# Optimization experiments

Measured on AMD Instinct MI355X. Metric: run time of the kernel, lower is better.

The kernel has to match this reference:

```python
import jax, jax.numpy as jnp
import numpy as np

B, S, D, H = 4, 2048, 1024, 16
DH = D // H  # depth per head


def setup_inputs() -> dict:
    key = jax.random.key(0)
    ks = jax.random.split(key, 12)
    s = 1.0 / np.sqrt(D)
    return {
        "v": jax.random.normal(ks[0], (B, S, D), jnp.float32),
        "k": jax.random.normal(ks[1], (B, S, D), jnp.float32),
        "q": jax.random.normal(ks[2], (B, S, D), jnp.float32),
        "mask": jnp.ones((B, 1, S, S), jnp.float32),
        "wq_w": jax.random.normal(ks[3], (D, D), jnp.float32) * s,
        "wq_b": jnp.zeros((D,), jnp.float32),
        "wk_w": jax.random.normal(ks[4], (D, D), jnp.float32) * s,
        "wk_b": jnp.zeros((D,), jnp.float32),
        "wv_w": jax.random.normal(ks[5], (D, D), jnp.float32) * s,
        "wv_b": jnp.zeros((D,), jnp.float32),
        "wo_w": jax.random.normal(ks[6], (D, D), jnp.float32) * s,
        "wo_b": jnp.zeros((D,), jnp.float32),
    }


def _split_heads(x):
    # [B, S, D] -> [B, H, S, DH]
    b, s, _ = x.shape
    return x.reshape(b, s, H, DH).transpose(0, 2, 1, 3)


def reference(v, k, q, mask, wq_w, wq_b, wk_w, wk_b, wv_w, wv_b, wo_w, wo_b):
    qh = _split_heads(q @ wq_w + wq_b)
    kh = _split_heads(k @ wk_w + wk_b)
    vh = _split_heads(v @ wv_w + wv_b)
    # scaled dot-product attention with multiplicative custom mask
    logits = jnp.einsum("bhqd,bhkd->bhqk", qh, kh) / jnp.sqrt(jnp.float32(DH))
    logits = logits * mask - 1e6 * (1.0 - mask)
    attn_weights = jax.nn.softmax(logits, axis=-1)
    ctx = jnp.einsum("bhqk,bhkd->bhqd", attn_weights, vh)
    concat = ctx.transpose(0, 2, 1, 3).reshape(-1, q.shape[1], D)
    out = concat @ wo_w + wo_b
    return out, attn_weights
```

## Files before the change

kernel.cpp:

```cpp
#include <hip/hip_runtime.h>


typedef unsigned short u16;
typedef unsigned int   u32;
typedef u16   u16x4  __attribute__((ext_vector_type(4)));
typedef u16   u16x8  __attribute__((ext_vector_type(8)));
typedef int   i32x4  __attribute__((ext_vector_type(4)));
typedef float f32x4  __attribute__((ext_vector_type(4)));
typedef __bf16 bf16x8 __attribute__((ext_vector_type(8)));

#define GLDS16(gp, lp)                                                         \
  __builtin_amdgcn_global_load_lds(                                            \
      (const __attribute__((address_space(1))) void*)(gp),                     \
      (__attribute__((address_space(3))) void*)(lp), 16, 0, 0)

__device__ __forceinline__ u16 f2bf(float x) {
  __bf16 h = (__bf16)x;
  union { __bf16 h; u16 u; } c; c.h = h; return c.u;
}

static const int Bn = 4, Sn = 2048, Dn = 1024, Hn = 16, DHn = 64;

__global__ __launch_bounds__(256) void cast3_k(const float* __restrict__ q,
                                               const float* __restrict__ k,
                                               const float* __restrict__ v,
                                               u16* __restrict__ out) {
  int which = blockIdx.x >> 12;
  size_t li = (size_t)(blockIdx.x & 4095) * 256 + threadIdx.x;
  const float* src = which == 0 ? q : which == 1 ? k : v;
  const f32x4* p = (const f32x4*)src + li * 2;
  f32x4 a = p[0], b = p[1];
  u16x8 r;
  r[0]=f2bf(a[0]); r[1]=f2bf(a[1]); r[2]=f2bf(a[2]); r[3]=f2bf(a[3]);
  r[4]=f2bf(b[0]); r[5]=f2bf(b[1]); r[6]=f2bf(b[2]); r[7]=f2bf(b[3]);
  *((u16x8*)(out + (size_t)which * 8388608) + li) = r;
}

__global__ __launch_bounds__(256) void castWT4_k(const float* __restrict__ w0,
                                                 const float* __restrict__ w1,
                                                 const float* __restrict__ w2,
                                                 const float* __restrict__ w3,
                                                 u16* __restrict__ WTb) {
  __shared__ u16 tile[64][72];
  int z = blockIdx.z;
  const float* W = z == 0 ? w0 : z == 1 ? w1 : z == 2 ? w2 : w3;
  u16* WT = WTb + (size_t)z * 1048576;
  int bx = blockIdx.x, by = blockIdx.y, t = threadIdx.x;
  for (int rr = 0; rr < 4; rr++) {
    int r = rr * 16 + (t >> 4);
    int c = (t & 15) * 4;
    float4 v = *(const float4*)(W + (size_t)(by * 64 + r) * 1024 + bx * 64 + c);
    tile[c + 0][r] = f2bf(v.x); tile[c + 1][r] = f2bf(v.y);
    tile[c + 2][r] = f2bf(v.z); tile[c + 3][r] = f2bf(v.w);
  }
  __syncthreads();
  for (int rr = 0; rr < 2; rr++) {
    int gid = rr * 256 + t;
    int r = gid >> 3, g = gid & 7;
    u16x8 v = *(const u16x8*)&tile[r][g * 8];
    *(u16x8*)(WT + (size_t)(bx * 64 + r) * 1024 + by * 64 + g * 8) = v;
  }
}

__global__ __launch_bounds__(256) void flags_k(const float* __restrict__ mask,
                                               int* __restrict__ flags) {
  __shared__ int ok_s;
  int t = threadIdx.x;
  if (t == 0) ok_s = 1;
  __syncthreads();
  int qt = blockIdx.x, kt = blockIdx.y, b = blockIdx.z;
  const float* base = mask + ((size_t)b * Sn + qt * 128) * Sn + kt * 64;
  int r = t >> 1, c0 = (t & 1) * 32;
  const float* p = base + (size_t)r * Sn + c0;
  bool ok = true;
  for (int i = 0; i < 8; i++) {
    float4 v = *(const float4*)(p + i * 4);
    ok = ok && (v.x == 1.0f) && (v.y == 1.0f) && (v.z == 1.0f) && (v.w == 1.0f);
  }
  if (!ok) atomicAnd(&ok_s, 0);
  __syncthreads();
  if (t == 0) flags[(b * 32 + kt) * 16 + qt] = ok_s;
}

__device__ __forceinline__ void gemm_body(const u16* __restrict__ A,
                                          const u16* __restrict__ BT,
                                          const float* __restrict__ bias,
                                          void* __restrict__ outp, int mode,
                                          int nt, int mt, char* sm) {
  const int K = 1024;
  int m0 = mt * 128, n0 = nt * 128;
  int tid = threadIdx.x, w = tid >> 6, l = tid & 63, l15 = l & 15, l4 = l >> 4;
  int wm = w >> 1, wn = w & 1;

  size_t goff_a[4], goff_b[4];
  int lbase[4];
  for (int i = 0; i < 4; i++) {
    int gi = (w * 4 + i) * 64 + l;
    int row = gi >> 3, g = gi & 7;
    int gx = g ^ (row & 7);
    goff_a[i] = (size_t)(m0 + row) * K + gx * 8;
    goff_b[i] = (size_t)(n0 + row) * K + gx * 8;
    lbase[i] = (w * 4 + i) * 1024;
  }

  f32x4 acc[4][4] = {};
  for (int t = 0; t < 16; t++) {
    int k0 = t * 64;
    for (int i = 0; i < 4; i++) {
      GLDS16(A + goff_a[i] + k0, sm + lbase[i]);
      GLDS16(BT + goff_b[i] + k0, sm + 16384 + lbase[i]);
    }
    __syncthreads();
#pragma unroll
    for (int kk = 0; kk < 2; kk++) {
      int kb = kk * 64 + l4 * 16;
      bf16x8 af[4], bf[4];
#pragma unroll
      for (int mi = 0; mi < 4; mi++) {
        int row = wm * 64 + mi * 16 + l15;
        af[mi] = *(const bf16x8*)(sm + row * 128 + (kb ^ ((row & 7) << 4)));
      }
#pragma unroll
      for (int nj = 0; nj < 4; nj++) {
        int row = wn * 64 + nj * 16 + l15;
        bf[nj] = *(const bf16x8*)(sm + 16384 + row * 128 + (kb ^ ((row & 7) << 4)));
      }
#pragma unroll
      for (int mi = 0; mi < 4; mi++)
#pragma unroll
        for (int nj = 0; nj < 4; nj++)
          acc[mi][nj] = __builtin_amdgcn_mfma_f32_16x16x32_bf16(af[mi], bf[nj], acc[mi][nj], 0, 0, 0);
    }
    __syncthreads();
  }

  if (mode == 3) {
    float* out = (float*)outp;
#pragma unroll
    for (int mi = 0; mi < 4; mi++)
#pragma unroll
      for (int nj = 0; nj < 4; nj++)
#pragma unroll
        for (int r = 0; r < 4; r++) {
          int mg = m0 + wm * 64 + mi * 16 + l4 * 4 + r;
          int ng = n0 + wn * 64 + nj * 16 + l15;
          out[(size_t)mg * 1024 + ng] = acc[mi][nj][r] + bias[ng];
        }
  } else if (mode == 2) {
    u16* vt = (u16*)outp;
#pragma unroll
    for (int mi = 0; mi < 4; mi++)
#pragma unroll
      for (int nj = 0; nj < 4; nj++) {
        int ng = n0 + wn * 64 + nj * 16 + l15;
        int h = ng >> 6, d = ng & 63;
        int mgb = m0 + wm * 64 + mi * 16 + l4 * 4;
        int b = mgb >> 11, s = mgb & 2047;
        float bs = bias[ng];
        u16x4 pk;
#pragma unroll
        for (int r = 0; r < 4; r++) pk[r] = f2bf(acc[mi][nj][r] + bs);
        *(u16x4*)(vt + ((size_t)(b * Hn + h) * DHn + d) * Sn + s) = pk;
      }
  } else {
    u16* oh = (u16*)outp;
    float sc = (mode == 0) ? 0.125f : 1.0f;
#pragma unroll
    for (int mi = 0; mi < 4; mi++)
#pragma unroll
      for (int nj = 0; nj < 4; nj++) {
        int ng = n0 + wn * 64 + nj * 16 + l15;
        int h = ng >> 6, d = ng & 63;
        float bs = bias[ng];
#pragma unroll
        for (int r = 0; r < 4; r++) {
          int mg = m0 + wm * 64 + mi * 16 + l4 * 4 + r;
          int b = mg >> 11, s = mg & 2047;
          oh[((size_t)(b * Hn + h) * Sn + s) * DHn + d] = f2bf((acc[mi][nj][r] + bs) * sc);
        }
      }
  }
}

__global__ __launch_bounds__(256) void gemmO_k(const u16* __restrict__ A,
                                               const u16* __restrict__ BT,
                                               const float* __restrict__ bias,
                                               float* __restrict__ outp) {
  __shared__ __align__(16) char sm[32768];
  int hw = blockIdx.x;
  int lg = (hw & 7) * 64 + (hw >> 3);
  int nt = lg & 7, mt = lg >> 3;
  gemm_body(A, BT, bias, (void*)outp, 3, nt, mt, sm);
}

__global__ __launch_bounds__(256) void gemm3_k(const u16* __restrict__ Ab,
                                               const u16* __restrict__ BTb,
                                               const float* __restrict__ b0,
                                               const float* __restrict__ b1,
                                               const float* __restrict__ b2,
                                               u16* __restrict__ outb) {
  __shared__ __align__(16) char sm[32768];
  int hw = blockIdx.x;
  int lg = (hw & 7) * 192 + (hw >> 3);
  int z = lg >> 9, r = lg & 511;
  int nt = r & 7, mt = r >> 3;
  const u16* A = Ab + (size_t)z * 8388608;
  const u16* BT = BTb + (size_t)z * 1048576;
  const float* bias = z == 0 ? b0 : z == 1 ? b1 : b2;
  u16* out = outb + (size_t)z * 8388608;
  gemm_body(A, BT, bias, (void*)out, z, nt, mt, sm);
}

#define K0_OFF 0
#define K1_OFF 8192
#define V0_OFF 16384
#define V1_OFF 24576
#define P_OFF  32768

__global__ __launch_bounds__(256) void attn_k(
    const u16* __restrict__ qh, const u16* __restrict__ kh,
    const u16* __restrict__ vt, const float* __restrict__ mask,
    const int* __restrict__ flags, float* __restrict__ attn,
    u16* __restrict__ ctxc) {
  __shared__ __align__(16) char sm[49152];
  int hw = blockIdx.x;
  int lg = (hw & 7) * 128 + (hw >> 3);
  int qt = lg & 15, h = (lg >> 4) & 15, b = lg >> 8;
  int bh = b * Hn + h;
  int tid = threadIdx.x, w = tid >> 6, l = tid & 63, l15 = l & 15, l4 = l >> 4;

  const u16* Qg = qh + ((size_t)bh * Sn + qt * 128) * DHn;
  const u16* Kg = kh + (size_t)bh * Sn * DHn;
  const u16* Vg = vt + (size_t)bh * DHn * Sn;
  const float* Mg = mask + (size_t)b * Sn * Sn + (size_t)(qt * 128) * Sn;

  u32 fl = (u32)__ballot(l < 32 && flags[(b * 32 + l) * 16 + qt] != 0);

  int srow[2], sgx8[2], sdst[2];
  for (int i = 0; i < 2; i++) {
    int gid = i * 256 + tid, row = gid >> 3, g = gid & 7;
    srow[i] = row; sgx8[i] = (g ^ (row & 7)) * 8; sdst[i] = gid * 16;
  }
#define STAGE_K(t, buf)                                                        \
  for (int i = 0; i < 2; i++)                                                  \
    GLDS16(Kg + (size_t)((t) * 64 + srow[i]) * DHn + sgx8[i], sm + (buf) + sdst[i]);
#define STAGE_V(t, buf)                                                        \
  for (int i = 0; i < 2; i++)                                                  \
    GLDS16(Vg + (size_t)srow[i] * Sn + (t) * 64 + sgx8[i], sm + (buf) + sdst[i]);

  bf16x8 qf[2][2];
#pragma unroll
  for (int ni = 0; ni < 2; ni++)
#pragma unroll
    for (int kk = 0; kk < 2; kk++)
      qf[ni][kk] = *(const bf16x8*)(Qg + (size_t)(w * 32 + ni * 16 + l15) * DHn + kk * 32 + l4 * 8);

  float m_run[2] = {-1e30f, -1e30f}, l_run[2] = {0.f, 0.f};

  STAGE_K(0, K0_OFF);
  for (int t = 0; t < 32; t++) {
    int kcur = (t & 1) ? K1_OFF : K0_OFF;
    __syncthreads();
    if (t < 31) { int knxt = (t & 1) ? K0_OFF : K1_OFF; STAGE_K(t + 1, knxt); }
    f32x4 s[4][2] = {};
#pragma unroll
    for (int kk = 0; kk < 2; kk++) {
      int kb = kk * 64 + l4 * 16;
      bf16x8 a[4];
#pragma unroll
      for (int mi = 0; mi < 4; mi++) {
        int row = mi * 16 + l15;
        a[mi] = *(const bf16x8*)(sm + kcur + row * 128 + (kb ^ ((row & 7) << 4)));
      }
#pragma unroll
      for (int mi = 0; mi < 4; mi++)
#pragma unroll
        for (int ni = 0; ni < 2; ni++)
          s[mi][ni] = __builtin_amdgcn_mfma_f32_16x16x32_bf16(a[mi], qf[ni][kk], s[mi][ni], 0, 0, 0);
    }
    if (!((fl >> t) & 1)) {
#pragma unroll
      for (int ni = 0; ni < 2; ni++) {
        const float* mrow = Mg + (size_t)(w * 32 + ni * 16 + l15) * Sn + t * 64;
#pragma unroll
        for (int mi = 0; mi < 4; mi++) {
          f32x4 mv = *(const f32x4*)(mrow + mi * 16 + l4 * 4);
#pragma unroll
          for (int r = 0; r < 4; r++)
            s[mi][ni][r] = s[mi][ni][r] * mv[r] - 1e6f * (1.f - mv[r]);
        }
      }
    }
#pragma unroll
    for (int ni = 0; ni < 2; ni++) {
      float tmax = -1e30f;
#pragma unroll
      for (int mi = 0; mi < 4; mi++)
#pragma unroll
        for (int r = 0; r < 4; r++) tmax = fmaxf(tmax, s[mi][ni][r]);
      tmax = fmaxf(tmax, __shfl_xor(tmax, 16));
      tmax = fmaxf(tmax, __shfl_xor(tmax, 32));
      float mn = fmaxf(m_run[ni], tmax);
      float sum = 0.f;
#pragma unroll
      for (int mi = 0; mi < 4; mi++)
#pragma unroll
        for (int r = 0; r < 4; r++) sum += __expf(s[mi][ni][r] - mn);
      sum += __shfl_xor(sum, 16);
      sum += __shfl_xor(sum, 32);
      l_run[ni] = l_run[ni] * __expf(m_run[ni] - mn) + sum;
      m_run[ni] = mn;
    }
  }
  float linv[2] = {1.f / l_run[0], 1.f / l_run[1]};

  f32x4 ctx[4][2] = {};
  STAGE_K(0, K0_OFF);
  STAGE_V(0, V0_OFF);
  for (int t = 0; t < 32; t++) {
    int kcur = (t & 1) ? K1_OFF : K0_OFF;
    int vcur = (t & 1) ? V1_OFF : V0_OFF;
    __syncthreads();
    if (t < 31) {
      int knxt = (t & 1) ? K0_OFF : K1_OFF;
      int vnxt = (t & 1) ? V0_OFF : V1_OFF;
      STAGE_K(t + 1, knxt);
      STAGE_V(t + 1, vnxt);
    }
    f32x4 s[4][2] = {};
#pragma unroll
    for (int kk = 0; kk < 2; kk++) {
      int kb = kk * 64 + l4 * 16;
      bf16x8 a[4];
#pragma unroll
      for (int mi = 0; mi < 4; mi++) {
        int row = mi * 16 + l15;
        a[mi] = *(const bf16x8*)(sm + kcur + row * 128 + (kb ^ ((row & 7) << 4)));
      }
#pragma unroll
      for (int mi = 0; mi < 4; mi++)
#pragma unroll
        for (int ni = 0; ni < 2; ni++)
          s[mi][ni] = __builtin_amdgcn_mfma_f32_16x16x32_bf16(a[mi], qf[ni][kk], s[mi][ni], 0, 0, 0);
    }
    if (!((fl >> t) & 1)) {
#pragma unroll
      for (int ni = 0; ni < 2; ni++) {
        const float* mrow = Mg + (size_t)(w * 32 + ni * 16 + l15) * Sn + t * 64;
#pragma unroll
        for (int mi = 0; mi < 4; mi++) {
          f32x4 mv = *(const f32x4*)(mrow + mi * 16 + l4 * 4);
#pragma unroll
          for (int r = 0; r < 4; r++)
            s[mi][ni][r] = s[mi][ni][r] * mv[r] - 1e6f * (1.f - mv[r]);
        }
      }
    }
#pragma unroll
    for (int ni = 0; ni < 2; ni++)
#pragma unroll
      for (int mi = 0; mi < 4; mi++)
#pragma unroll
        for (int r = 0; r < 4; r++) s[mi][ni][r] = __expf(s[mi][ni][r] - m_run[ni]);
#pragma unroll
    for (int ni = 0; ni < 2; ni++) {
      float* arow = attn + ((size_t)bh * Sn + qt * 128 + w * 32 + ni * 16 + l15) * Sn + t * 64;
#pragma unroll
      for (int mi = 0; mi < 4; mi++) {
        f32x4 o;
#pragma unroll
        for (int r = 0; r < 4; r++) o[r] = s[mi][ni][r] * linv[ni];
        *(f32x4*)(arow + mi * 16 + l4 * 4) = o;
      }
    }
#pragma unroll
    for (int ni = 0; ni < 2; ni++) {
      int q = w * 32 + ni * 16 + l15;
#pragma unroll
      for (int mi = 0; mi < 4; mi++) {
        u16x4 pk;
#pragma unroll
        for (int r = 0; r < 4; r++) pk[r] = f2bf(s[mi][ni][r]);
        int kb = mi * 32 + l4 * 8;
        *(u16x4*)(sm + P_OFF + q * 128 + (kb ^ ((q & 7) << 4))) = pk;
      }
    }
#pragma unroll
    for (int kk = 0; kk < 2; kk++) {
      int kb = kk * 64 + l4 * 16;
      bf16x8 av[4], bp[2];
#pragma unroll
      for (int mi = 0; mi < 4; mi++) {
        int row = mi * 16 + l15;
        av[mi] = *(const bf16x8*)(sm + vcur + row * 128 + (kb ^ ((row & 7) << 4)));
      }
#pragma unroll
      for (int ni = 0; ni < 2; ni++) {
        int q = w * 32 + ni * 16 + l15;
        bp[ni] = *(const bf16x8*)(sm + P_OFF + q * 128 + (kb ^ ((q & 7) << 4)));
      }
#pragma unroll
      for (int mi = 0; mi < 4; mi++)
#pragma unroll
        for (int ni = 0; ni < 2; ni++)
          ctx[mi][ni] = __builtin_amdgcn_mfma_f32_16x16x32_bf16(av[mi], bp[ni], ctx[mi][ni], 0, 0, 0);
    }
  }

#pragma unroll
  for (int ni = 0; ni < 2; ni++) {
    int q = w * 32 + ni * 16 + l15;
#pragma unroll
    for (int mi = 0; mi < 4; mi++) {
      u16x4 ck;
#pragma unroll
      for (int r = 0; r < 4; r++) ck[r] = f2bf(ctx[mi][ni][r] * linv[ni]);
      int db = mi * 32 + l4 * 8;
      *(u16x4*)(sm + P_OFF + q * 128 + (db ^ ((q & 7) << 4))) = ck;
    }
  }
  __syncthreads();
  {
    int q = tid >> 1, hf = tid & 1;
    u16* dst = ctxc + ((size_t)b * Sn + qt * 128 + q) * Dn + h * DHn + hf * 32;
#pragma unroll
    for (int c4 = 0; c4 < 4; c4++) {
      int db = hf * 64 + c4 * 16;
      i32x4 v = *(const i32x4*)(sm + P_OFF + q * 128 + (db ^ ((q & 7) << 4)));
      *(i32x4*)(dst + c4 * 8) = v;
    }
  }
}

extern "C" void kernel_launch(void* const* d_in, const int* in_sizes, int n_in,
                              void* d_out, int out_size, void* d_ws, size_t ws_size,
                              hipStream_t stream) {
  const float* v_f  = (const float*)d_in[0];
  const float* k_f  = (const float*)d_in[1];
  const float* q_f  = (const float*)d_in[2];
  const float* mask = (const float*)d_in[3];
  const float* wq_w = (const float*)d_in[4];
  const float* wq_b = (const float*)d_in[5];
  const float* wk_w = (const float*)d_in[6];
  const float* wk_b = (const float*)d_in[7];
  const float* wv_w = (const float*)d_in[8];
  const float* wv_b = (const float*)d_in[9];
  const float* wo_w = (const float*)d_in[10];
  const float* wo_b = (const float*)d_in[11];

  char* ws = (char*)d_ws;
  u16*   qbf  = (u16*)(ws + 0);
  u16*   wT   = (u16*)(ws + 50331648);
  u16*   woT  = (u16*)(ws + 56623104);
  u16*   qhp  = (u16*)(ws + 58720256);
  u16*   khp  = (u16*)(ws + 75497472);
  u16*   vtp  = (u16*)(ws + 92274688);
  u16*   ctxc = (u16*)(ws + 109051904);
  int*   flg  = (int*)(ws + 125829120);

  float* out  = (float*)d_out;
  float* attn = out + (size_t)Bn * Sn * Dn;

  cast3_k<<<12288, 256, 0, stream>>>(q_f, k_f, v_f, qbf);
  castWT4_k<<<dim3(16, 16, 4), 256, 0, stream>>>(wq_w, wk_w, wv_w, wo_w, wT);
  flags_k<<<dim3(16, 32, 4), 256, 0, stream>>>(mask, flg);

  gemm3_k<<<1536, 256, 0, stream>>>(qbf, wT, wq_b, wk_b, wv_b, qhp);

  attn_k<<<1024, 256, 0, stream>>>(qhp, khp, vtp, mask, flg, attn, ctxc);

  gemmO_k<<<512, 256, 0, stream>>>(ctxc, woT, wo_b, out);
}
```

Before: 628.4 us.

## Split attention into separate log-sum pass and output pass with exp2 and no max

```diff
diff --git a/kernel.cpp b/kernel.cpp
--- a/kernel.cpp
+++ b/kernel.cpp
@@ -20,6 +20,7 @@
 }
 
 static const int Bn = 4, Sn = 2048, Dn = 1024, Hn = 16, DHn = 64;
+#define MASK_NEG (-1442695.0f)
 
 __global__ __launch_bounds__(256) void cast3_k(const float* __restrict__ q,
                                                const float* __restrict__ k,
@@ -164,7 +165,7 @@
       }
   } else {
     u16* oh = (u16*)outp;
-    float sc = (mode == 0) ? 0.125f : 1.0f;
+    float sc = (mode == 0) ? 0.18033688f : 1.0f;
 #pragma unroll
     for (int mi = 0; mi < 4; mi++)
 #pragma unroll
@@ -211,17 +212,109 @@
   gemm_body(A, BT, bias, (void*)out, z, nt, mt, sm);
 }
 
+__global__ __launch_bounds__(256) void pass1_k(
+    const u16* __restrict__ qh, const u16* __restrict__ kh,
+    const float* __restrict__ mask, const int* __restrict__ flags,
+    float* __restrict__ cvec) {
+  __shared__ __align__(16) char sm[32768];
+  int hw = blockIdx.x;
+  int lg = (hw & 7) * 128 + (hw >> 3);
+  int qt = lg & 15, h = (lg >> 4) & 15, b = lg >> 8;
+  int bh = b * Hn + h;
+  int tid = threadIdx.x, w = tid >> 6, l = tid & 63, l15 = l & 15, l4 = l >> 4;
+
+  const u16* Qg = qh + ((size_t)bh * Sn + qt * 128) * DHn;
+  const u16* Kg = kh + (size_t)bh * Sn * DHn;
+  const float* Mg = mask + (size_t)b * Sn * Sn + (size_t)(qt * 128) * Sn;
+
+  u32 fl = (u32)__ballot(l < 32 && flags[(b * 32 + l) * 16 + qt] != 0);
+
+  int srow[4], sgx8[4], sdst[4];
+  for (int i = 0; i < 4; i++) {
+    int gid = i * 256 + tid, row = gid >> 3, g = gid & 7;
+    srow[i] = row; sgx8[i] = (g ^ (row & 7)) * 8; sdst[i] = gid * 16;
+  }
+#define STAGE_K128(t, buf)                                                     \
+  for (int i = 0; i < 4; i++)                                                  \
+    GLDS16(Kg + (size_t)((t) * 128 + srow[i]) * DHn + sgx8[i], sm + (buf) + sdst[i]);
+
+  bf16x8 qf[2][2];
+#pragma unroll
+  for (int ni = 0; ni < 2; ni++)
+#pragma unroll
+    for (int kk = 0; kk < 2; kk++)
+      qf[ni][kk] = *(const bf16x8*)(Qg + (size_t)(w * 32 + ni * 16 + l15) * DHn + kk * 32 + l4 * 8);
+
+  float lsum[2] = {0.f, 0.f};
+
+  STAGE_K128(0, 0);
+  for (int t = 0; t < 16; t++) {
+    int kcur = (t & 1) ? 16384 : 0;
+    __syncthreads();
+    if (t < 15) { int knxt = (t & 1) ? 0 : 16384; STAGE_K128(t + 1, knxt); }
+#pragma unroll
+    for (int h2 = 0; h2 < 2; h2++) {
+      int kt = t * 2 + h2;
+      f32x4 s[4][2] = {};
+#pragma unroll
+      for (int kk = 0; kk < 2; kk++) {
+        int kb = kk * 64 + l4 * 16;
+        bf16x8 a[4];
+#pragma unroll
+        for (int mi = 0; mi < 4; mi++) {
+          int row = h2 * 64 + mi * 16 + l15;
+          a[mi] = *(const bf16x8*)(sm + kcur + row * 128 + (kb ^ ((row & 7) << 4)));
+        }
+#pragma unroll
+        for (int mi = 0; mi < 4; mi++)
+#pragma unroll
+          for (int ni = 0; ni < 2; ni++)
+            s[mi][ni] = __builtin_amdgcn_mfma_f32_16x16x32_bf16(a[mi], qf[ni][kk], s[mi][ni], 0, 0, 0);
+      }
+      if (!((fl >> kt) & 1)) {
+#pragma unroll
+        for (int ni = 0; ni < 2; ni++) {
+          const float* mrow = Mg + (size_t)(w * 32 + ni * 16 + l15) * Sn + kt * 64;
+#pragma unroll
+          for (int mi = 0; mi < 4; mi++) {
+            f32x4 mv = *(const f32x4*)(mrow + mi * 16 + l4 * 4);
+#pragma unroll
+            for (int r = 0; r < 4; r++)
+              s[mi][ni][r] = s[mi][ni][r] * mv[r] + MASK_NEG * (1.f - mv[r]);
+          }
+        }
+      }
+#pragma unroll
+      for (int ni = 0; ni < 2; ni++)
+#pragma unroll
+        for (int mi = 0; mi < 4; mi++)
+#pragma unroll
+          for (int r = 0; r < 4; r++) lsum[ni] += __builtin_exp2f(s[mi][ni][r]);
+    }
+  }
+#pragma unroll
+  for (int ni = 0; ni < 2; ni++) {
+    lsum[ni] += __shfl_xor(lsum[ni], 16);
+    lsum[ni] += __shfl_xor(lsum[ni], 32);
+  }
+  if (l4 == 0) {
+#pragma unroll
+    for (int ni = 0; ni < 2; ni++)
+      cvec[(size_t)bh * Sn + qt * 128 + w * 32 + ni * 16 + l15] = __builtin_log2f(lsum[ni]);
+  }
+}
+
 #define K0_OFF 0
 #define K1_OFF 8192
 #define V0_OFF 16384
 #define V1_OFF 24576
 #define P_OFF  32768
 
-__global__ __launch_bounds__(256) void attn_k(
+__global__ __launch_bounds__(256) void pass2_k(
     const u16* __restrict__ qh, const u16* __restrict__ kh,
     const u16* __restrict__ vt, const float* __restrict__ mask,
-    const int* __restrict__ flags, float* __restrict__ attn,
-    u16* __restrict__ ctxc) {
+    const int* __restrict__ flags, const float* __restrict__ cvec,
+    float* __restrict__ attn, u16* __restrict__ ctxc) {
   __shared__ __align__(16) char sm[49152];
   int hw = blockIdx.x;
   int lg = (hw & 7) * 128 + (hw >> 3);
@@ -236,6 +329,11 @@
 
   u32 fl = (u32)__ballot(l < 32 && flags[(b * 32 + l) * 16 + qt] != 0);
 
+  float cv[2];
+#pragma unroll
+  for (int ni = 0; ni < 2; ni++)
+    cv[ni] = cvec[(size_t)bh * Sn + qt * 128 + w * 32 + ni * 16 + l15];
+
   int srow[2], sgx8[2], sdst[2];
   for (int i = 0; i < 2; i++) {
     int gid = i * 256 + tid, row = gid >> 3, g = gid & 7;
@@ -254,65 +352,6 @@
 #pragma unroll
     for (int kk = 0; kk < 2; kk++)
       qf[ni][kk] = *(const bf16x8*)(Qg + (size_t)(w * 32 + ni * 16 + l15) * DHn + kk * 32 + l4 * 8);
-
-  float m_run[2] = {-1e30f, -1e30f}, l_run[2] = {0.f, 0.f};
-
-  STAGE_K(0, K0_OFF);
-  for (int t = 0; t < 32; t++) {
-    int kcur = (t & 1) ? K1_OFF : K0_OFF;
-    __syncthreads();
-    if (t < 31) { int knxt = (t & 1) ? K0_OFF : K1_OFF; STAGE_K(t + 1, knxt); }
-    f32x4 s[4][2] = {};
-#pragma unroll
-    for (int kk = 0; kk < 2; kk++) {
-      int kb = kk * 64 + l4 * 16;
-      bf16x8 a[4];
-#pragma unroll
-      for (int mi = 0; mi < 4; mi++) {
-        int row = mi * 16 + l15;
-        a[mi] = *(const bf16x8*)(sm + kcur + row * 128 + (kb ^ ((row & 7) << 4)));
-      }
-#pragma unroll
-      for (int mi = 0; mi < 4; mi++)
-#pragma unroll
-        for (int ni = 0; ni < 2; ni++)
-          s[mi][ni] = __builtin_amdgcn_mfma_f32_16x16x32_bf16(a[mi], qf[ni][kk], s[mi][ni], 0, 0, 0);
-    }
-    if (!((fl >> t) & 1)) {
-#pragma unroll
-      for (int ni = 0; ni < 2; ni++) {
-        const float* mrow = Mg + (size_t)(w * 32 + ni * 16 + l15) * Sn + t * 64;
-#pragma unroll
-        for (int mi = 0; mi < 4; mi++) {
-          f32x4 mv = *(const f32x4*)(mrow + mi * 16 + l4 * 4);
-#pragma unroll
-          for (int r = 0; r < 4; r++)
-            s[mi][ni][r] = s[mi][ni][r] * mv[r] - 1e6f * (1.f - mv[r]);
-        }
-      }
-    }
-#pragma unroll
-    for (int ni = 0; ni < 2; ni++) {
-      float tmax = -1e30f;
-#pragma unroll
-      for (int mi = 0; mi < 4; mi++)
-#pragma unroll
-        for (int r = 0; r < 4; r++) tmax = fmaxf(tmax, s[mi][ni][r]);
-      tmax = fmaxf(tmax, __shfl_xor(tmax, 16));
-      tmax = fmaxf(tmax, __shfl_xor(tmax, 32));
-      float mn = fmaxf(m_run[ni], tmax);
-      float sum = 0.f;
-#pragma unroll
-      for (int mi = 0; mi < 4; mi++)
-#pragma unroll
-        for (int r = 0; r < 4; r++) sum += __expf(s[mi][ni][r] - mn);
-      sum += __shfl_xor(sum, 16);
-      sum += __shfl_xor(sum, 32);
-      l_run[ni] = l_run[ni] * __expf(m_run[ni] - mn) + sum;
-      m_run[ni] = mn;
-    }
-  }
-  float linv[2] = {1.f / l_run[0], 1.f / l_run[1]};
 
   f32x4 ctx[4][2] = {};
   STAGE_K(0, K0_OFF);
@@ -352,7 +391,7 @@
           f32x4 mv = *(const f32x4*)(mrow + mi * 16 + l4 * 4);
 #pragma unroll
           for (int r = 0; r < 4; r++)
-            s[mi][ni][r] = s[mi][ni][r] * mv[r] - 1e6f * (1.f - mv[r]);
+            s[mi][ni][r] = s[mi][ni][r] * mv[r] + MASK_NEG * (1.f - mv[r]);
         }
       }
     }
@@ -361,17 +400,13 @@
 #pragma unroll
       for (int mi = 0; mi < 4; mi++)
 #pragma unroll
-        for (int r = 0; r < 4; r++) s[mi][ni][r] = __expf(s[mi][ni][r] - m_run[ni]);
+        for (int r = 0; r < 4; r++) s[mi][ni][r] = __builtin_exp2f(s[mi][ni][r] - cv[ni]);
 #pragma unroll
     for (int ni = 0; ni < 2; ni++) {
       float* arow = attn + ((size_t)bh * Sn + qt * 128 + w * 32 + ni * 16 + l15) * Sn + t * 64;
 #pragma unroll
-      for (int mi = 0; mi < 4; mi++) {
-        f32x4 o;
-#pragma unroll
-        for (int r = 0; r < 4; r++) o[r] = s[mi][ni][r] * linv[ni];
-        *(f32x4*)(arow + mi * 16 + l4 * 4) = o;
-      }
+      for (int mi = 0; mi < 4; mi++)
+        *(f32x4*)(arow + mi * 16 + l4 * 4) = s[mi][ni];
     }
 #pragma unroll
     for (int ni = 0; ni < 2; ni++) {
@@ -414,7 +449,7 @@
     for (int mi = 0; mi < 4; mi++) {
       u16x4 ck;
 #pragma unroll
-      for (int r = 0; r < 4; r++) ck[r] = f2bf(ctx[mi][ni][r] * linv[ni]);
+      for (int r = 0; r < 4; r++) ck[r] = f2bf(ctx[mi][ni][r]);
       int db = mi * 32 + l4 * 8;
       *(u16x4*)(sm + P_OFF + q * 128 + (db ^ ((q & 7) << 4))) = ck;
     }
@@ -456,7 +491,8 @@
   u16*   khp  = (u16*)(ws + 75497472);
   u16*   vtp  = (u16*)(ws + 92274688);
   u16*   ctxc = (u16*)(ws + 109051904);
-  int*   flg  = (int*)(ws + 125829120);
+  float* cvec = (float*)(ws + 125829120);
+  int*   flg  = (int*)(ws + 126353408);
 
   float* out  = (float*)d_out;
   float* attn = out + (size_t)Bn * Sn * Dn;
@@ -467,7 +503,8 @@
 
   gemm3_k<<<1536, 256, 0, stream>>>(qbf, wT, wq_b, wk_b, wv_b, qhp);
 
-  attn_k<<<1024, 256, 0, stream>>>(qhp, khp, vtp, mask, flg, attn, ctxc);
+  pass1_k<<<1024, 256, 0, stream>>>(qhp, khp, mask, flg, cvec);
+  pass2_k<<<1024, 256, 0, stream>>>(qhp, khp, vtp, mask, flg, cvec, attn, ctxc);
 
   gemmO_k<<<512, 256, 0, stream>>>(ctxc, woT, wo_b, out);
 }
```

Result: slower. 651.5 us (+3.7%).
